# Performance work log

Measured on AMD Instinct MI355X. Metric: run time of the kernel, lower is better.

## Reference

```python
import math
import jax, jax.numpy as jnp
import numpy as np

D, NH, NL, NP = 256, 8, 3, 4
HD = D // NH
SHAPES = np.array([[92, 92], [46, 46], [23, 23]], dtype=np.int32)
LSI = np.concatenate([[0], np.cumsum(SHAPES[:, 0] * SHAPES[:, 1])[:-1]]).astype(np.int32)
LV = int((SHAPES[:, 0] * SHAPES[:, 1]).sum())  # 11109
B, LQ = 2, LV


def setup_inputs() -> dict:
    key = jax.random.key(0)
    ks = jax.random.split(key, 8)
    query = jax.random.normal(ks[0], (B, LQ, D), jnp.float32)
    reference_points = jax.random.uniform(ks[1], (B, LQ, NL, 2), dtype=jnp.float32)
    value_flat = jax.random.normal(ks[2], (B, LV, D), jnp.float32)
    # sampling_offsets: small random weight + structured directional bias (as in _reset_parameters)
    W_off = jax.random.normal(ks[3], (D, NH * NL * NP * 2), jnp.float32) * 0.01
    thetas = np.arange(NH, dtype=np.float64) * (2.0 * math.pi / NH)
    g = np.stack([np.cos(thetas), np.sin(thetas)], axis=-1)
    g = g / np.abs(g).max(axis=-1, keepdims=True)
    g = np.tile(g[:, None, None, :], (1, NL, NP, 1))
    g = g * (np.arange(NP) + 1)[None, None, :, None]
    b_off = jnp.asarray(g.reshape(-1), jnp.float32)
    W_attn = jax.random.normal(ks[4], (D, NH * NL * NP), jnp.float32) * 0.01
    b_attn = jnp.zeros((NH * NL * NP,), jnp.float32)
    W_val = jax.random.normal(ks[5], (D, D), jnp.float32) * (1.0 / math.sqrt(D))
    b_val = jnp.zeros((D,), jnp.float32)
    W_out = jax.random.normal(ks[6], (D, D), jnp.float32) * (1.0 / math.sqrt(D))
    b_out = jnp.zeros((D,), jnp.float32)
    return dict(query=query, reference_points=reference_points, value_flat=value_flat,
                W_val=W_val, b_val=b_val, W_off=W_off, b_off=b_off,
                W_attn=W_attn, b_attn=b_attn, W_out=W_out, b_out=b_out,
                spatial_shapes=jnp.asarray(SHAPES), level_start_index=jnp.asarray(LSI))


def _bilinear_sample(val_l, grid):
    """torch.F.grid_sample(mode='bilinear', padding_mode='zeros', align_corners=False).
    val_l: [B,H,W,nH,hd]; grid: [B,Q,nH,P,2] with (x,y) in [-1,1].
    Returns [B,nH,Q,P,hd]."""
    Bq, H, W, nH, hd = val_l.shape
    Q, P = grid.shape[1], grid.shape[3]
    x = ((grid[..., 0] + 1.0) * W - 1.0) * 0.5   # pixel coords, align_corners=False
    y = ((grid[..., 1] + 1.0) * H - 1.0) * 0.5
    x0f, y0f = jnp.floor(x), jnp.floor(y)
    lx, ly = x - x0f, y - y0f
    x0, y0 = x0f.astype(jnp.int32), y0f.astype(jnp.int32)
    val_bh = val_l.transpose(0, 3, 1, 2, 4).reshape(Bq * nH, H * W, hd)

    def corner(yi, xi, w):
        valid = (xi >= 0) & (xi < W) & (yi >= 0) & (yi < H)
        idx = jnp.clip(yi, 0, H - 1) * W + jnp.clip(xi, 0, W - 1)   # [B,Q,nH,P]
        idx_bh = idx.transpose(0, 2, 1, 3).reshape(Bq * nH, Q * P)
        g = jnp.take_along_axis(val_bh, idx_bh[:, :, None], axis=1)  # [B*nH, Q*P, hd]
        wm = (w * valid.astype(w.dtype)).transpose(0, 2, 1, 3).reshape(Bq * nH, Q * P, 1)
        return g * wm

    out = (corner(y0, x0, (1 - ly) * (1 - lx)) + corner(y0, x0 + 1, (1 - ly) * lx)
           + corner(y0 + 1, x0, ly * (1 - lx)) + corner(y0 + 1, x0 + 1, ly * lx))
    return out.reshape(Bq, nH, Q, P, hd)


def reference(query, reference_points, value_flat, W_val, b_val, W_off, b_off,
              W_attn, b_attn, W_out, b_out, spatial_shapes, level_start_index):
    shapes = np.asarray(spatial_shapes)          # static level geometry
    starts = np.asarray(level_start_index)
    Bq, Lq, _ = query.shape
    value = (value_flat @ W_val + b_val).reshape(Bq, -1, NH, HD)
    off = (query @ W_off + b_off).reshape(Bq, Lq, NH, NL, NP, 2)        # (dy,dx) pixels
    aw = jax.nn.softmax((query @ W_attn + b_attn).reshape(Bq, Lq, NH, NL * NP), axis=-1)
    aw = aw.reshape(Bq, Lq, NH, NL, NP)
    sh_f = jnp.asarray(shapes, jnp.float32)                              # [L,2] = (H,W)
    norm_off = off / sh_f[None, None, None, :, None, :]
    loc = reference_points[:, :, None, :, None, :] + norm_off           # [B,Lq,NH,NL,NP,2] (y,x)
    grid = 2.0 * loc[..., ::-1] - 1.0                                    # (x,y) in [-1,1]
    out = jnp.zeros((Bq, Lq, NH, HD), query.dtype)
    for l in range(NL):
        H, W = int(shapes[l, 0]), int(shapes[l, 1])
        s = int(starts[l])
        val_l = value[:, s:s + H * W].reshape(Bq, H, W, NH, HD)
        sampled = _bilinear_sample(val_l, grid[:, :, :, l])              # [B,NH,Lq,NP,HD]
        out = out + jnp.einsum('bhqpc,bqhp->bqhc', sampled, aw[:, :, :, l])
    return out.reshape(Bq, Lq, D) @ W_out + b_out
```

## Files before the change

### kernel.cpp

```cpp
#include <hip/hip_runtime.h>

#define LQn   11109
#define Bn    2
#define MTOT  (Bn * LQn)

typedef __attribute__((ext_vector_type(8))) short short8;
typedef __attribute__((ext_vector_type(4))) float f32x4;

__device__ __forceinline__ unsigned short f2bf(float f) {
  union { float f; unsigned int u; } v; v.f = f;
  unsigned int r = v.u + 0x7fffu + ((v.u >> 16) & 1u);
  return (unsigned short)(r >> 16);
}

__global__ __launch_bounds__(256) void prep_weights(
    const float* __restrict__ Wval, const float* __restrict__ Woff,
    const float* __restrict__ Wattn, const float* __restrict__ Wout,
    const float* __restrict__ boff, const float* __restrict__ battn,
    unsigned short* __restrict__ Wval_t, unsigned short* __restrict__ Wcat_t,
    unsigned short* __restrict__ Wout_t, float* __restrict__ bcat) {
  int i = blockIdx.x * 256 + threadIdx.x;
  int n = i >> 8, k = i & 255;
  if (n < 256) {
    Wval_t[i] = f2bf(Wval[k * 256 + n]);
    Wout_t[i] = f2bf(Wout[k * 256 + n]);
  }
  float src = (n < 192) ? Woff[k * 192 + n] : Wattn[k * 96 + (n - 192)];
  Wcat_t[i] = f2bf(src);
  if (i < 288) bcat[i] = (i < 192) ? boff[i] : battn[i - 192];
}

__global__ __launch_bounds__(256) void gemm_fused12(
    const float* __restrict__ Aval,
    const float* __restrict__ Aq,
    const unsigned short* __restrict__ Bval,
    const unsigned short* __restrict__ Bcat,
    const float* __restrict__ bval, const float* __restrict__ bcat,
    unsigned short* __restrict__ value16,
    float* __restrict__ logits) {
  __shared__ unsigned short As[64][40];
  __shared__ unsigned short Bs[64][40];

  const int bm = blockIdx.x;
  int bn = blockIdx.y;
  const bool is2 = bn >= 4;
  if (is2) bn -= 4;
  const float* __restrict__ A = is2 ? Aq : Aval;
  const unsigned short* __restrict__ Bt = is2 ? Bcat : Bval;
  const float* __restrict__ bias = is2 ? bcat : bval;
  const int N = is2 ? 288 : 256;

  const int t = threadIdx.x;
  const int wave = t >> 6, lane = t & 63;
  const int wm = wave >> 1, wn = wave & 1;
  const int quad = lane >> 4, l16 = lane & 15;

  const int ldr = t >> 2;
  const int ldk = (t & 3) * 8;
  const int arow = bm * 64 + ldr;
  const int brow = bn * 64 + ldr;

  f32x4 acc[2][2];
  for (int i = 0; i < 2; i++)
    for (int j = 0; j < 2; j++) acc[i][j] = (f32x4){0.f, 0.f, 0.f, 0.f};

  for (int kb = 0; kb < 8; kb++) {
    const int k0 = kb * 32;
    float4 a0 = {0.f, 0.f, 0.f, 0.f}, a1 = a0;
    uint4 bv = {0u, 0u, 0u, 0u};
    if (arow < MTOT) {
      a0 = *(const float4*)(A + (size_t)arow * 256 + k0 + ldk);
      a1 = *(const float4*)(A + (size_t)arow * 256 + k0 + ldk + 4);
    }
    if (brow < N) bv = *(const uint4*)(Bt + (size_t)brow * 256 + k0 + ldk);
    ushort4 lo, hi;
    lo.x = f2bf(a0.x); lo.y = f2bf(a0.y); lo.z = f2bf(a0.z); lo.w = f2bf(a0.w);
    hi.x = f2bf(a1.x); hi.y = f2bf(a1.y); hi.z = f2bf(a1.z); hi.w = f2bf(a1.w);
    __syncthreads();
    *(ushort4*)(&As[ldr][ldk]) = lo;
    *(ushort4*)(&As[ldr][ldk + 4]) = hi;
    *(uint4*)(&Bs[ldr][ldk]) = bv;
    __syncthreads();
    short8 af[2], bfr[2];
    for (int i = 0; i < 2; i++)
      af[i] = *(const short8*)(&As[wm * 32 + i * 16 + l16][quad * 8]);
    for (int j = 0; j < 2; j++)
      bfr[j] = *(const short8*)(&Bs[wn * 32 + j * 16 + l16][quad * 8]);
    for (int i = 0; i < 2; i++)
      for (int j = 0; j < 2; j++)
        acc[i][j] = __builtin_amdgcn_mfma_f32_16x16x32_bf16(af[i], bfr[j], acc[i][j], 0, 0, 0);
  }

  for (int i = 0; i < 2; i++)
    for (int j = 0; j < 2; j++) {
      int colg = bn * 64 + wn * 32 + j * 16 + l16;
      if (colg >= N) continue;
      float bsv = bias[colg];
      int row0 = bm * 64 + wm * 32 + i * 16 + quad * 4;
      for (int r = 0; r < 4; r++) {
        int rg = row0 + r;
        if (rg >= MTOT) continue;
        float v = acc[i][j][r] + bsv;
        if (is2) {
          logits[(size_t)rg * 288 + colg] = v;
        } else {
          int b = (rg >= LQn) ? 1 : 0;
          int p = rg - b * LQn;
          value16[((size_t)(b * 8 + (colg >> 5)) * LQn + p) * 32 + (colg & 31)] = f2bf(v);
        }
      }
    }
}

__global__ __launch_bounds__(256) void gemm_a16(
    const unsigned short* __restrict__ A,
    const unsigned short* __restrict__ Bt,
    const float* __restrict__ bias,
    float* __restrict__ C) {
  __shared__ unsigned short As[64][40];
  __shared__ unsigned short Bs[64][40];

  const int t = threadIdx.x;
  const int bm = blockIdx.x, bn = blockIdx.y;
  const int wave = t >> 6, lane = t & 63;
  const int wm = wave >> 1, wn = wave & 1;
  const int quad = lane >> 4, l16 = lane & 15;

  const int ldr = t >> 2;
  const int ldk = (t & 3) * 8;
  const int arow = bm * 64 + ldr;
  const int brow = bn * 64 + ldr;

  f32x4 acc[2][2];
  for (int i = 0; i < 2; i++)
    for (int j = 0; j < 2; j++) acc[i][j] = (f32x4){0.f, 0.f, 0.f, 0.f};

  for (int kb = 0; kb < 8; kb++) {
    const int k0 = kb * 32;
    uint4 av = {0u, 0u, 0u, 0u}, bv = {0u, 0u, 0u, 0u};
    if (arow < MTOT) av = *(const uint4*)(A + (size_t)arow * 256 + k0 + ldk);
    bv = *(const uint4*)(Bt + (size_t)brow * 256 + k0 + ldk);
    __syncthreads();
    *(uint4*)(&As[ldr][ldk]) = av;
    *(uint4*)(&Bs[ldr][ldk]) = bv;
    __syncthreads();
    short8 af[2], bfr[2];
    for (int i = 0; i < 2; i++)
      af[i] = *(const short8*)(&As[wm * 32 + i * 16 + l16][quad * 8]);
    for (int j = 0; j < 2; j++)
      bfr[j] = *(const short8*)(&Bs[wn * 32 + j * 16 + l16][quad * 8]);
    for (int i = 0; i < 2; i++)
      for (int j = 0; j < 2; j++)
        acc[i][j] = __builtin_amdgcn_mfma_f32_16x16x32_bf16(af[i], bfr[j], acc[i][j], 0, 0, 0);
  }

  for (int i = 0; i < 2; i++)
    for (int j = 0; j < 2; j++) {
      int colg = bn * 64 + wn * 32 + j * 16 + l16;
      float bsv = bias[colg];
      int row0 = bm * 64 + wm * 32 + i * 16 + quad * 4;
      for (int r = 0; r < 4; r++) {
        int rg = row0 + r;
        if (rg < MTOT) C[(size_t)rg * 256 + colg] = acc[i][j][r] + bsv;
      }
    }
}

__global__ __launch_bounds__(256) void msda_sample3(
    const unsigned short* __restrict__ value16,
    const float* __restrict__ logits,
    const float* __restrict__ refp,
    unsigned short* __restrict__ sampled) {
  __shared__ float lg[4][288];
  __shared__ float rfs[4][6];
  __shared__ float hmx[4][8], hrd[4][8];
  __shared__ float tw[4][96][4];
  __shared__ unsigned int ti[4][96][4];

  const int t = threadIdx.x;
  const int ql = t >> 6;
  const int lane = t & 63;
  const int bq = blockIdx.x * 4 + ql;
  const bool qv = bq < MTOT;

  if (qv) {
    for (int i = lane; i < 288; i += 64) lg[ql][i] = logits[(size_t)bq * 288 + i];
    if (lane < 6) rfs[ql][lane] = refp[(size_t)bq * 6 + lane];
  }
  __syncthreads();

  if (qv && lane < 8) {
    float mx = -1e30f;
#pragma unroll
    for (int i = 0; i < 12; i++) mx = fmaxf(mx, lg[ql][192 + lane * 12 + i]);
    float den = 0.f;
#pragma unroll
    for (int i = 0; i < 12; i++) den += __expf(lg[ql][192 + lane * 12 + i] - mx);
    hmx[ql][lane] = mx;
    hrd[ql][lane] = 1.0f / den;
  }
  __syncthreads();

  if (qv) {
    const int Hs[3] = {92, 46, 23};
    const int Ss[3] = {0, 8464, 10580};
#pragma unroll
    for (int rnd = 0; rnd < 2; rnd++) {
      const int s = lane + rnd * 64;
      if (s < 96) {
        const int h = s / 12;
        const int pl = s - h * 12;
        const int l = pl >> 2;
        const int H = Hs[l], W = Hs[l], S = Ss[l];
        const float aw = __expf(lg[ql][192 + s] - hmx[ql][h]) * hrd[ql][h];
        const float offy = lg[ql][2 * s], offx = lg[ql][2 * s + 1];
        const float x = rfs[ql][l * 2 + 1] * W + offx - 0.5f;
        const float y = rfs[ql][l * 2 + 0] * H + offy - 0.5f;
        const float xf = floorf(x), yf = floorf(y);
        const int x0 = (int)xf, y0 = (int)yf;
        const float lx = x - xf, ly = y - yf;
        const bool xv0 = (x0 >= 0) & (x0 < W), xv1 = (x0 + 1 >= 0) & (x0 + 1 < W);
        const bool yv0 = (y0 >= 0) & (y0 < H), yv1 = (y0 + 1 >= 0) & (y0 + 1 < H);
        const int xc0 = min(max(x0, 0), W - 1), xc1 = min(max(x0 + 1, 0), W - 1);
        const int yc0 = min(max(y0, 0), H - 1), yc1 = min(max(y0 + 1, 0), H - 1);
        ti[ql][s][0] = (unsigned)(S + yc0 * W + xc0) << 6;
        ti[ql][s][1] = (unsigned)(S + yc0 * W + xc1) << 6;
        ti[ql][s][2] = (unsigned)(S + yc1 * W + xc0) << 6;
        ti[ql][s][3] = (unsigned)(S + yc1 * W + xc1) << 6;
        tw[ql][s][0] = (yv0 & xv0) ? aw * (1.f - ly) * (1.f - lx) : 0.f;
        tw[ql][s][1] = (yv0 & xv1) ? aw * (1.f - ly) * lx : 0.f;
        tw[ql][s][2] = (yv1 & xv0) ? aw * ly * (1.f - lx) : 0.f;
        tw[ql][s][3] = (yv1 & xv1) ? aw * ly * lx : 0.f;
      }
    }
  }
  __syncthreads();

  if (qv) {
    const int h = lane >> 3, cg = lane & 7;
    const unsigned laneoff = (unsigned)h * (LQn * 64u) + (unsigned)cg * 8u;
    const char* __restrict__ vb =
        (const char*)(value16 + (size_t)(bq / LQn) * (8u * LQn * 32u));
    float a0 = 0.f, a1 = 0.f, a2 = 0.f, a3 = 0.f;
#pragma unroll
    for (int p = 0; p < 12; p++) {
      const int s = h * 12 + p;
      const f32x4 wv = *(const f32x4*)(&tw[ql][s][0]);
      const uint4 iv = *(const uint4*)(&ti[ql][s][0]);
#pragma unroll
      for (int k = 0; k < 4; k++) {
        const unsigned tib = (k == 0) ? iv.x : (k == 1) ? iv.y : (k == 2) ? iv.z : iv.w;
        const float w = wv[k];
        const uint2 u = *(const uint2*)(vb + (laneoff + tib));
        a0 += w * __uint_as_float(u.x << 16);
        a1 += w * __uint_as_float(u.x & 0xffff0000u);
        a2 += w * __uint_as_float(u.y << 16);
        a3 += w * __uint_as_float(u.y & 0xffff0000u);
      }
    }
    ushort4 o;
    o.x = f2bf(a0); o.y = f2bf(a1); o.z = f2bf(a2); o.w = f2bf(a3);
    *(ushort4*)(sampled + (size_t)bq * 256 + h * 32 + cg * 4) = o;
  }
}

extern "C" void kernel_launch(void* const* d_in, const int* in_sizes, int n_in,
                              void* d_out, int out_size, void* d_ws, size_t ws_size,
                              hipStream_t stream) {
  const float* query      = (const float*)d_in[0];
  const float* refp       = (const float*)d_in[1];
  const float* value_flat = (const float*)d_in[2];
  const float* W_val      = (const float*)d_in[3];
  const float* b_val      = (const float*)d_in[4];
  const float* W_off      = (const float*)d_in[5];
  const float* b_off      = (const float*)d_in[6];
  const float* W_attn     = (const float*)d_in[7];
  const float* b_attn     = (const float*)d_in[8];
  const float* W_out      = (const float*)d_in[9];
  const float* b_out      = (const float*)d_in[10];

  char* w = (char*)d_ws;
  size_t o = 0;
  auto carve = [&](size_t bytes) -> void* {
    void* p = (void*)(w + o);
    o += (bytes + 255) & ~(size_t)255;
    return p;
  };
  unsigned short* Wval_t  = (unsigned short*)carve(256 * 256 * 2);
  unsigned short* Wcat_t  = (unsigned short*)carve(288 * 256 * 2);
  unsigned short* Wout_t  = (unsigned short*)carve(256 * 256 * 2);
  float*          bcat    = (float*)carve(288 * 4);
  unsigned short* value16 = (unsigned short*)carve((size_t)MTOT * 256 * 2);
  float*          logits  = (float*)carve((size_t)MTOT * 288 * 4);
  unsigned short* samp_bf = (unsigned short*)carve((size_t)MTOT * 256 * 2);

  prep_weights<<<288, 256, 0, stream>>>(W_val, W_off, W_attn, W_out, b_off, b_attn,
                                        Wval_t, Wcat_t, Wout_t, bcat);

  const int mg = (MTOT + 63) / 64;
  dim3 g12(mg, 9);
  gemm_fused12<<<g12, 256, 0, stream>>>(value_flat, query, Wval_t, Wcat_t,
                                        b_val, bcat, value16, logits);

  const int sgrid = (MTOT + 3) / 4;
  msda_sample3<<<sgrid, 256, 0, stream>>>(value16, logits, refp, samp_bf);

  dim3 g3(mg, 4);
  gemm_a16<<<g3, 256, 0, stream>>>(samp_bf, Wout_t, b_out, (float*)d_out);
}
```

Baseline: 195.0 us.

## Use 128x128 GEMM tiles with direct global-to-LDS loads and a separate bf16 pre-cast

```diff
diff --git a/kernel.cpp b/kernel.cpp
--- a/kernel.cpp
+++ b/kernel.cpp
@@ -1,8 +1,7 @@
 #include <hip/hip_runtime.h>
 
 #define LQn   11109
-#define Bn    2
-#define MTOT  (Bn * LQn)
+#define MTOT  22218
 
 typedef __attribute__((ext_vector_type(8))) short short8;
 typedef __attribute__((ext_vector_type(4))) float f32x4;
@@ -11,6 +10,30 @@
   union { float f; unsigned int u; } v; v.f = f;
   unsigned int r = v.u + 0x7fffu + ((v.u >> 16) & 1u);
   return (unsigned short)(r >> 16);
+}
+
+__device__ __forceinline__ void g2l16(const void* g, void* l) {
+  __builtin_amdgcn_global_load_lds(
+      (const __attribute__((address_space(1))) unsigned int*)g,
+      (__attribute__((address_space(3))) unsigned int*)l, 16, 0, 0);
+}
+
+__global__ __launch_bounds__(256) void cast_both(
+    const float* __restrict__ q, const float* __restrict__ v,
+    unsigned short* __restrict__ qb, unsigned short* __restrict__ vb) {
+  const int n8 = MTOT * 256 / 8;
+  int i = blockIdx.x * 256 + threadIdx.x;
+  const float* src; unsigned short* dst; int j;
+  if (i < n8) { src = q; dst = qb; j = i; }
+  else        { src = v; dst = vb; j = i - n8; }
+  if (j >= n8) return;
+  float4 a = ((const float4*)src)[j * 2];
+  float4 b = ((const float4*)src)[j * 2 + 1];
+  ushort4 lo, hi;
+  lo.x = f2bf(a.x); lo.y = f2bf(a.y); lo.z = f2bf(a.z); lo.w = f2bf(a.w);
+  hi.x = f2bf(b.x); hi.y = f2bf(b.y); hi.z = f2bf(b.z); hi.w = f2bf(b.w);
+  ((ushort4*)dst)[j * 2] = lo;
+  ((ushort4*)dst)[j * 2 + 1] = hi;
 }
 
 __global__ __launch_bounds__(256) void prep_weights(
@@ -25,145 +48,140 @@
     Wval_t[i] = f2bf(Wval[k * 256 + n]);
     Wout_t[i] = f2bf(Wout[k * 256 + n]);
   }
-  float src = (n < 192) ? Woff[k * 192 + n] : Wattn[k * 96 + (n - 192)];
+  float src = (n < 192) ? Woff[k * 192 + n] : (n < 288 ? Wattn[k * 96 + (n - 192)] : 0.f);
   Wcat_t[i] = f2bf(src);
-  if (i < 288) bcat[i] = (i < 192) ? boff[i] : battn[i - 192];
-}
-
-__global__ __launch_bounds__(256) void gemm_fused12(
-    const float* __restrict__ Aval,
-    const float* __restrict__ Aq,
-    const unsigned short* __restrict__ Bval,
-    const unsigned short* __restrict__ Bcat,
+  if (i < 384) bcat[i] = (i < 192) ? boff[i] : (i < 288 ? battn[i - 192] : 0.f);
+}
+
+__device__ __forceinline__ void gemm128_loop(
+    const unsigned short* __restrict__ A, int Arow0,
+    const unsigned short* __restrict__ Bt, int Brow0,
+    unsigned short* As, unsigned short* Bs, f32x4 (&acc)[4][4]) {
+  const int t = threadIdx.x;
+  const int w = t >> 6, lane = t & 63;
+  const int rowl = lane >> 2;
+  const int kby = (lane & 3) * 16;
+  const int quad = lane >> 4, l16 = lane & 15;
+  const int wm = w >> 1, wn = w & 1;
+
+#pragma unroll 1
+  for (int kb = 0; kb < 8; kb++) {
+    if (kb) __syncthreads();
+#pragma unroll
+    for (int i16 = 0; i16 < 2; i16++) {
+      int r = w * 32 + i16 * 16 + rowl;
+      int ga = Arow0 + r; ga = (ga < MTOT) ? ga : (MTOT - 1);
+      g2l16((const char*)A + (size_t)ga * 512 + kb * 64 + kby,
+            (char*)As + w * 2048 + i16 * 1024);
+      g2l16((const char*)Bt + (size_t)(Brow0 + r) * 512 + kb * 64 + kby,
+            (char*)Bs + w * 2048 + i16 * 1024);
+    }
+    __syncthreads();
+    short8 af[4], bfr[4];
+#pragma unroll
+    for (int i = 0; i < 4; i++)
+      af[i] = *(const short8*)((const char*)As + (wm * 64 + i * 16 + l16) * 64 + quad * 16);
+#pragma unroll
+    for (int j = 0; j < 4; j++)
+      bfr[j] = *(const short8*)((const char*)Bs + (wn * 64 + j * 16 + l16) * 64 + quad * 16);
+#pragma unroll
+    for (int i = 0; i < 4; i++)
+#pragma unroll
+      for (int j = 0; j < 4; j++)
+        acc[i][j] = __builtin_amdgcn_mfma_f32_16x16x32_bf16(af[i], bfr[j], acc[i][j], 0, 0, 0);
+  }
+}
+
+__global__ __launch_bounds__(256) void gemm128_12(
+    const unsigned short* __restrict__ Av, const unsigned short* __restrict__ Aq,
+    const unsigned short* __restrict__ Bv, const unsigned short* __restrict__ Bc,
     const float* __restrict__ bval, const float* __restrict__ bcat,
-    unsigned short* __restrict__ value16,
-    float* __restrict__ logits) {
-  __shared__ unsigned short As[64][40];
-  __shared__ unsigned short Bs[64][40];
-
+    unsigned short* __restrict__ value16, float* __restrict__ logits) {
+  __shared__ unsigned short As[128 * 32];
+  __shared__ unsigned short Bs[128 * 32];
   const int bm = blockIdx.x;
-  int bn = blockIdx.y;
-  const bool is2 = bn >= 4;
-  if (is2) bn -= 4;
-  const float* __restrict__ A = is2 ? Aq : Aval;
-  const unsigned short* __restrict__ Bt = is2 ? Bcat : Bval;
-  const float* __restrict__ bias = is2 ? bcat : bval;
-  const int N = is2 ? 288 : 256;
-
-  const int t = threadIdx.x;
-  const int wave = t >> 6, lane = t & 63;
-  const int wm = wave >> 1, wn = wave & 1;
+  const int bn = blockIdx.y;
+  const bool is2 = bn >= 2;
+  const int bnl = is2 ? bn - 2 : bn;
+
+  f32x4 acc[4][4];
+  for (int i = 0; i < 4; i++)
+    for (int j = 0; j < 4; j++) acc[i][j] = (f32x4){0.f, 0.f, 0.f, 0.f};
+
+  gemm128_loop(is2 ? Aq : Av, bm * 128, is2 ? Bc : Bv, bnl * 128, As, Bs, acc);
+
+  const int t = threadIdx.x, lane = t & 63;
   const int quad = lane >> 4, l16 = lane & 15;
-
-  const int ldr = t >> 2;
-  const int ldk = (t & 3) * 8;
-  const int arow = bm * 64 + ldr;
-  const int brow = bn * 64 + ldr;
-
-  f32x4 acc[2][2];
-  for (int i = 0; i < 2; i++)
-    for (int j = 0; j < 2; j++) acc[i][j] = (f32x4){0.f, 0.f, 0.f, 0.f};
-
-  for (int kb = 0; kb < 8; kb++) {
-    const int k0 = kb * 32;
-    float4 a0 = {0.f, 0.f, 0.f, 0.f}, a1 = a0;
-    uint4 bv = {0u, 0u, 0u, 0u};
-    if (arow < MTOT) {
-      a0 = *(const float4*)(A + (size_t)arow * 256 + k0 + ldk);
-      a1 = *(const float4*)(A + (size_t)arow * 256 + k0 + ldk + 4);
-    }
-    if (brow < N) bv = *(const uint4*)(Bt + (size_t)brow * 256 + k0 + ldk);
-    ushort4 lo, hi;
-    lo.x = f2bf(a0.x); lo.y = f2bf(a0.y); lo.z = f2bf(a0.z); lo.w = f2bf(a0.w);
-    hi.x = f2bf(a1.x); hi.y = f2bf(a1.y); hi.z = f2bf(a1.z); hi.w = f2bf(a1.w);
-    __syncthreads();
-    *(ushort4*)(&As[ldr][ldk]) = lo;
-    *(ushort4*)(&As[ldr][ldk + 4]) = hi;
-    *(uint4*)(&Bs[ldr][ldk]) = bv;
-    __syncthreads();
-    short8 af[2], bfr[2];
-    for (int i = 0; i < 2; i++)
-      af[i] = *(const short8*)(&As[wm * 32 + i * 16 + l16][quad * 8]);
-    for (int j = 0; j < 2; j++)
-      bfr[j] = *(const short8*)(&Bs[wn * 32 + j * 16 + l16][quad * 8]);
-    for (int i = 0; i < 2; i++)
-      for (int j = 0; j < 2; j++)
-        acc[i][j] = __builtin_amdgcn_mfma_f32_16x16x32_bf16(af[i], bfr[j], acc[i][j], 0, 0, 0);
-  }
-
-  for (int i = 0; i < 2; i++)
-    for (int j = 0; j < 2; j++) {
-      int colg = bn * 64 + wn * 32 + j * 16 + l16;
-      if (colg >= N) continue;
-      float bsv = bias[colg];
-      int row0 = bm * 64 + wm * 32 + i * 16 + quad * 4;
+  const int wm = t >> 7, wn = (t >> 6) & 1;
+
+  if (!is2) {
+#pragma unroll
+    for (int j = 0; j < 4; j++) {
+      const int col = bnl * 128 + wn * 64 + j * 16 + l16;
+      const float bs = bval[col];
+      const int hbase = col >> 5, cch = col & 31;
+#pragma unroll
+      for (int i = 0; i < 4; i++) {
+        const int row0 = bm * 128 + wm * 64 + i * 16 + quad * 4;
+#pragma unroll
+        for (int r = 0; r < 4; r++) {
+          const int rg = row0 + r;
+          if (rg >= MTOT) continue;
+          const int b = rg >= LQn ? 1 : 0;
+          const int p = rg - b * LQn;
+          value16[((size_t)(b * 8 + hbase) * LQn + p) * 32 + cch] = f2bf(acc[i][j][r] + bs);
+        }
+      }
+    }
+  } else {
+#pragma unroll
+    for (int j = 0; j < 4; j++) {
+      const int col = bnl * 128 + wn * 64 + j * 16 + l16;
+      if (col >= 288) continue;
+      const float bs = bcat[col];
+#pragma unroll
+      for (int i = 0; i < 4; i++) {
+        const int row0 = bm * 128 + wm * 64 + i * 16 + quad * 4;
+#pragma unroll
+        for (int r = 0; r < 4; r++) {
+          const int rg = row0 + r;
+          if (rg < MTOT) logits[(size_t)rg * 288 + col] = acc[i][j][r] + bs;
+        }
+      }
+    }
+  }
+}
+
+__global__ __launch_bounds__(256) void gemm128_out(
+    const unsigned short* __restrict__ A, const unsigned short* __restrict__ Bt,
+    const float* __restrict__ bias, float* __restrict__ C) {
+  __shared__ unsigned short As[128 * 32];
+  __shared__ unsigned short Bs[128 * 32];
+  const int bm = blockIdx.x, bn = blockIdx.y;
+
+  f32x4 acc[4][4];
+  for (int i = 0; i < 4; i++)
+    for (int j = 0; j < 4; j++) acc[i][j] = (f32x4){0.f, 0.f, 0.f, 0.f};
+
+  gemm128_loop(A, bm * 128, Bt, bn * 128, As, Bs, acc);
+
+  const int t = threadIdx.x, lane = t & 63;
+  const int quad = lane >> 4, l16 = lane & 15;
+  const int wm = t >> 7, wn = (t >> 6) & 1;
+#pragma unroll
+  for (int j = 0; j < 4; j++) {
+    const int col = bn * 128 + wn * 64 + j * 16 + l16;
+    const float bs = bias[col];
+#pragma unroll
+    for (int i = 0; i < 4; i++) {
+      const int row0 = bm * 128 + wm * 64 + i * 16 + quad * 4;
+#pragma unroll
       for (int r = 0; r < 4; r++) {
-        int rg = row0 + r;
-        if (rg >= MTOT) continue;
-        float v = acc[i][j][r] + bsv;
-        if (is2) {
-          logits[(size_t)rg * 288 + colg] = v;
-        } else {
-          int b = (rg >= LQn) ? 1 : 0;
-          int p = rg - b * LQn;
-          value16[((size_t)(b * 8 + (colg >> 5)) * LQn + p) * 32 + (colg & 31)] = f2bf(v);
-        }
-      }
-    }
-}
-
-__global__ __launch_bounds__(256) void gemm_a16(
-    const unsigned short* __restrict__ A,
-    const unsigned short* __restrict__ Bt,
-    const float* __restrict__ bias,
-    float* __restrict__ C) {
-  __shared__ unsigned short As[64][40];
-  __shared__ unsigned short Bs[64][40];
-
-  const int t = threadIdx.x;
-  const int bm = blockIdx.x, bn = blockIdx.y;
-  const int wave = t >> 6, lane = t & 63;
-  const int wm = wave >> 1, wn = wave & 1;
-  const int quad = lane >> 4, l16 = lane & 15;
-
-  const int ldr = t >> 2;
-  const int ldk = (t & 3) * 8;
-  const int arow = bm * 64 + ldr;
-  const int brow = bn * 64 + ldr;
-
-  f32x4 acc[2][2];
-  for (int i = 0; i < 2; i++)
-    for (int j = 0; j < 2; j++) acc[i][j] = (f32x4){0.f, 0.f, 0.f, 0.f};
-
-  for (int kb = 0; kb < 8; kb++) {
-    const int k0 = kb * 32;
-    uint4 av = {0u, 0u, 0u, 0u}, bv = {0u, 0u, 0u, 0u};
-    if (arow < MTOT) av = *(const uint4*)(A + (size_t)arow * 256 + k0 + ldk);
-    bv = *(const uint4*)(Bt + (size_t)brow * 256 + k0 + ldk);
-    __syncthreads();
-    *(uint4*)(&As[ldr][ldk]) = av;
-    *(uint4*)(&Bs[ldr][ldk]) = bv;
-    __syncthreads();
-    short8 af[2], bfr[2];
-    for (int i = 0; i < 2; i++)
-      af[i] = *(const short8*)(&As[wm * 32 + i * 16 + l16][quad * 8]);
-    for (int j = 0; j < 2; j++)
-      bfr[j] = *(const short8*)(&Bs[wn * 32 + j * 16 + l16][quad * 8]);
-    for (int i = 0; i < 2; i++)
-      for (int j = 0; j < 2; j++)
-        acc[i][j] = __builtin_amdgcn_mfma_f32_16x16x32_bf16(af[i], bfr[j], acc[i][j], 0, 0, 0);
-  }
-
-  for (int i = 0; i < 2; i++)
-    for (int j = 0; j < 2; j++) {
-      int colg = bn * 64 + wn * 32 + j * 16 + l16;
-      float bsv = bias[colg];
-      int row0 = bm * 64 + wm * 32 + i * 16 + quad * 4;
-      for (int r = 0; r < 4; r++) {
-        int rg = row0 + r;
-        if (rg < MTOT) C[(size_t)rg * 256 + colg] = acc[i][j][r] + bsv;
-      }
-    }
+        const int rg = row0 + r;
+        if (rg < MTOT) C[(size_t)rg * 256 + col] = acc[i][j][r] + bs;
+      }
+    }
+  }
 }
 
 __global__ __launch_bounds__(256) void msda_sample3(
@@ -286,25 +304,29 @@
     o += (bytes + 255) & ~(size_t)255;
     return p;
   };
+  unsigned short* q_bf    = (unsigned short*)carve((size_t)MTOT * 256 * 2);
+  unsigned short* v_bf    = (unsigned short*)carve((size_t)MTOT * 256 * 2);
   unsigned short* Wval_t  = (unsigned short*)carve(256 * 256 * 2);
-  unsigned short* Wcat_t  = (unsigned short*)carve(288 * 256 * 2);
+  unsigned short* Wcat_t  = (unsigned short*)carve(384 * 256 * 2);
   unsigned short* Wout_t  = (unsigned short*)carve(256 * 256 * 2);
-  float*          bcat    = (float*)carve(288 * 4);
+  float*          bcat    = (float*)carve(384 * 4);
   unsigned short* value16 = (unsigned short*)carve((size_t)MTOT * 256 * 2);
   float*          logits  = (float*)carve((size_t)MTOT * 288 * 4);
   unsigned short* samp_bf = (unsigned short*)carve((size_t)MTOT * 256 * 2);
 
-  prep_weights<<<288, 256, 0, stream>>>(W_val, W_off, W_attn, W_out, b_off, b_attn,
+  const int n8x2 = 2 * (MTOT * 256 / 8);
+  cast_both<<<(n8x2 + 255) / 256, 256, 0, stream>>>(query, value_flat, q_bf, v_bf);
+  prep_weights<<<384, 256, 0, stream>>>(W_val, W_off, W_attn, W_out, b_off, b_attn,
                                         Wval_t, Wcat_t, Wout_t, bcat);
 
-  const int mg = (MTOT + 63) / 64;
-  dim3 g12(mg, 9);
-  gemm_fused12<<<g12, 256, 0, stream>>>(value_flat, query, Wval_t, Wcat_t,
-                                        b_val, bcat, value16, logits);
+  const int mg = (MTOT + 127) / 128;
+  dim3 g12(mg, 5);
+  gemm128_12<<<g12, 256, 0, stream>>>(v_bf, q_bf, Wval_t, Wcat_t,
+                                      b_val, bcat, value16, logits);
 
   const int sgrid = (MTOT + 3) / 4;
   msda_sample3<<<sgrid, 256, 0, stream>>>(value16, logits, refp, samp_bf);
 
-  dim3 g3(mg, 4);
-  gemm_a16<<<g3, 256, 0, stream>>>(samp_bf, Wout_t, b_out, (float*)d_out);
-}
+  dim3 g3(mg, 2);
+  gemm128_out<<<g3, 256, 0, stream>>>(samp_bf, Wout_t, b_out, (float*)d_out);
+}
```

Measured after the change: 204.8 us. 5.1% more time.

## Process eight queries per block with 16-byte gathers and spread sampling setup

Applied to the files above, without the earlier changes.

```diff
diff --git a/kernel.cpp b/kernel.cpp
--- a/kernel.cpp
+++ b/kernel.cpp
@@ -1,8 +1,7 @@
 #include <hip/hip_runtime.h>
 
 #define LQn   11109
-#define Bn    2
-#define MTOT  (Bn * LQn)
+#define MTOT  22218
 
 typedef __attribute__((ext_vector_type(8))) short short8;
 typedef __attribute__((ext_vector_type(4))) float f32x4;
@@ -166,56 +165,58 @@
     }
 }
 
-__global__ __launch_bounds__(256) void msda_sample3(
+__global__ __launch_bounds__(256) void msda_sample4(
     const unsigned short* __restrict__ value16,
     const float* __restrict__ logits,
     const float* __restrict__ refp,
     unsigned short* __restrict__ sampled) {
-  __shared__ float lg[4][288];
-  __shared__ float rfs[4][6];
-  __shared__ float hmx[4][8], hrd[4][8];
-  __shared__ float tw[4][96][4];
-  __shared__ unsigned int ti[4][96][4];
+  __shared__ float          tw[8][96][4];
+  __shared__ unsigned short ti[8][96][4];
+  __shared__ float hmx[8][8], hrd[8][8];
+  __shared__ float rfs[8][6];
 
   const int t = threadIdx.x;
-  const int ql = t >> 6;
-  const int lane = t & 63;
-  const int bq = blockIdx.x * 4 + ql;
-  const bool qv = bq < MTOT;
-
-  if (qv) {
-    for (int i = lane; i < 288; i += 64) lg[ql][i] = logits[(size_t)bq * 288 + i];
-    if (lane < 6) rfs[ql][lane] = refp[(size_t)bq * 6 + lane];
+  const int qbase = blockIdx.x * 8;
+
+  if (t < 48) {
+    int q = t / 6;
+    if (qbase + q < MTOT) rfs[q][t - q * 6] = refp[(size_t)qbase * 6 + t];
+  }
+  if (t >= 64 && t < 128) {
+    int tt = t - 64;
+    int q = tt >> 3, h = tt & 7;
+    int bq = qbase + q;
+    if (bq < MTOT) {
+      const float* lrow = logits + (size_t)bq * 288 + 192 + h * 12;
+      float mx = -1e30f;
+#pragma unroll
+      for (int i = 0; i < 12; i++) mx = fmaxf(mx, lrow[i]);
+      float den = 0.f;
+#pragma unroll
+      for (int i = 0; i < 12; i++) den += __expf(lrow[i] - mx);
+      hmx[q][h] = mx;
+      hrd[q][h] = 1.0f / den;
+    }
   }
   __syncthreads();
 
-  if (qv && lane < 8) {
-    float mx = -1e30f;
-#pragma unroll
-    for (int i = 0; i < 12; i++) mx = fmaxf(mx, lg[ql][192 + lane * 12 + i]);
-    float den = 0.f;
-#pragma unroll
-    for (int i = 0; i < 12; i++) den += __expf(lg[ql][192 + lane * 12 + i] - mx);
-    hmx[ql][lane] = mx;
-    hrd[ql][lane] = 1.0f / den;
-  }
-  __syncthreads();
-
-  if (qv) {
+  {
     const int Hs[3] = {92, 46, 23};
     const int Ss[3] = {0, 8464, 10580};
 #pragma unroll
-    for (int rnd = 0; rnd < 2; rnd++) {
-      const int s = lane + rnd * 64;
-      if (s < 96) {
-        const int h = s / 12;
-        const int pl = s - h * 12;
+    for (int r = 0; r < 3; r++) {
+      const int task = t + r * 256;
+      const int q = task / 96, s = task - q * 96;
+      const int bq = qbase + q;
+      if (bq < MTOT) {
+        const int h = s / 12, pl = s - h * 12;
         const int l = pl >> 2;
         const int H = Hs[l], W = Hs[l], S = Ss[l];
-        const float aw = __expf(lg[ql][192 + s] - hmx[ql][h]) * hrd[ql][h];
-        const float offy = lg[ql][2 * s], offx = lg[ql][2 * s + 1];
-        const float x = rfs[ql][l * 2 + 1] * W + offx - 0.5f;
-        const float y = rfs[ql][l * 2 + 0] * H + offy - 0.5f;
+        const float* lrow = logits + (size_t)bq * 288;
+        const float aw = __expf(lrow[192 + s] - hmx[q][h]) * hrd[q][h];
+        const float offy = lrow[2 * s], offx = lrow[2 * s + 1];
+        const float x = rfs[q][l * 2 + 1] * W + offx - 0.5f;
+        const float y = rfs[q][l * 2 + 0] * H + offy - 0.5f;
         const float xf = floorf(x), yf = floorf(y);
         const int x0 = (int)xf, y0 = (int)yf;
         const float lx = x - xf, ly = y - yf;
@@ -223,44 +224,62 @@
         const bool yv0 = (y0 >= 0) & (y0 < H), yv1 = (y0 + 1 >= 0) & (y0 + 1 < H);
         const int xc0 = min(max(x0, 0), W - 1), xc1 = min(max(x0 + 1, 0), W - 1);
         const int yc0 = min(max(y0, 0), H - 1), yc1 = min(max(y0 + 1, 0), H - 1);
-        ti[ql][s][0] = (unsigned)(S + yc0 * W + xc0) << 6;
-        ti[ql][s][1] = (unsigned)(S + yc0 * W + xc1) << 6;
-        ti[ql][s][2] = (unsigned)(S + yc1 * W + xc0) << 6;
-        ti[ql][s][3] = (unsigned)(S + yc1 * W + xc1) << 6;
-        tw[ql][s][0] = (yv0 & xv0) ? aw * (1.f - ly) * (1.f - lx) : 0.f;
-        tw[ql][s][1] = (yv0 & xv1) ? aw * (1.f - ly) * lx : 0.f;
-        tw[ql][s][2] = (yv1 & xv0) ? aw * ly * (1.f - lx) : 0.f;
-        tw[ql][s][3] = (yv1 & xv1) ? aw * ly * lx : 0.f;
+        const int slot = pl * 8 + h;
+        ti[q][slot][0] = (unsigned short)(S + yc0 * W + xc0);
+        ti[q][slot][1] = (unsigned short)(S + yc0 * W + xc1);
+        ti[q][slot][2] = (unsigned short)(S + yc1 * W + xc0);
+        ti[q][slot][3] = (unsigned short)(S + yc1 * W + xc1);
+        tw[q][slot][0] = (yv0 & xv0) ? aw * (1.f - ly) * (1.f - lx) : 0.f;
+        tw[q][slot][1] = (yv0 & xv1) ? aw * (1.f - ly) * lx : 0.f;
+        tw[q][slot][2] = (yv1 & xv0) ? aw * ly * (1.f - lx) : 0.f;
+        tw[q][slot][3] = (yv1 & xv1) ? aw * ly * lx : 0.f;
       }
     }
   }
   __syncthreads();
 
-  if (qv) {
-    const int h = lane >> 3, cg = lane & 7;
-    const unsigned laneoff = (unsigned)h * (LQn * 64u) + (unsigned)cg * 8u;
+  {
+    const int w = t >> 6, lane = t & 63;
+    const int q = w * 2 + (lane >> 5);
+    const int h = (lane >> 2) & 7, cg = lane & 3;
+    const int bq = qbase + q;
+    const bool qv = bq < MTOT;
+    const int bqc = qv ? bq : 0;
     const char* __restrict__ vb =
-        (const char*)(value16 + (size_t)(bq / LQn) * (8u * LQn * 32u));
+        (const char*)value16 + (size_t)(bqc / LQn) * ((size_t)LQn * 512);
+    const unsigned laneoff = (unsigned)h * (LQn * 64u) + (unsigned)cg * 16u;
+
     float a0 = 0.f, a1 = 0.f, a2 = 0.f, a3 = 0.f;
+    float a4 = 0.f, a5 = 0.f, a6 = 0.f, a7 = 0.f;
 #pragma unroll
     for (int p = 0; p < 12; p++) {
-      const int s = h * 12 + p;
-      const f32x4 wv = *(const f32x4*)(&tw[ql][s][0]);
-      const uint4 iv = *(const uint4*)(&ti[ql][s][0]);
+      const int slot = p * 8 + h;
+      const ushort4 tiv = *(const ushort4*)(&ti[q][slot][0]);
+      const f32x4 wv = *(const f32x4*)(&tw[q][slot][0]);
 #pragma unroll
       for (int k = 0; k < 4; k++) {
-        const unsigned tib = (k == 0) ? iv.x : (k == 1) ? iv.y : (k == 2) ? iv.z : iv.w;
-        const float w = wv[k];
-        const uint2 u = *(const uint2*)(vb + (laneoff + tib));
-        a0 += w * __uint_as_float(u.x << 16);
-        a1 += w * __uint_as_float(u.x & 0xffff0000u);
-        a2 += w * __uint_as_float(u.y << 16);
-        a3 += w * __uint_as_float(u.y & 0xffff0000u);
+        const unsigned pix =
+            (k == 0) ? tiv.x : (k == 1) ? tiv.y : (k == 2) ? tiv.z : tiv.w;
+        const float wgt = wv[k];
+        const uint4 u = *(const uint4*)(vb + ((pix << 6) + laneoff));
+        a0 += wgt * __uint_as_float(u.x << 16);
+        a1 += wgt * __uint_as_float(u.x & 0xffff0000u);
+        a2 += wgt * __uint_as_float(u.y << 16);
+        a3 += wgt * __uint_as_float(u.y & 0xffff0000u);
+        a4 += wgt * __uint_as_float(u.z << 16);
+        a5 += wgt * __uint_as_float(u.z & 0xffff0000u);
+        a6 += wgt * __uint_as_float(u.w << 16);
+        a7 += wgt * __uint_as_float(u.w & 0xffff0000u);
       }
     }
-    ushort4 o;
-    o.x = f2bf(a0); o.y = f2bf(a1); o.z = f2bf(a2); o.w = f2bf(a3);
-    *(ushort4*)(sampled + (size_t)bq * 256 + h * 32 + cg * 4) = o;
+    if (qv) {
+      uint4 o;
+      o.x = (unsigned)f2bf(a0) | ((unsigned)f2bf(a1) << 16);
+      o.y = (unsigned)f2bf(a2) | ((unsigned)f2bf(a3) << 16);
+      o.z = (unsigned)f2bf(a4) | ((unsigned)f2bf(a5) << 16);
+      o.w = (unsigned)f2bf(a6) | ((unsigned)f2bf(a7) << 16);
+      *(uint4*)(sampled + (size_t)bq * 256 + h * 32 + cg * 8) = o;
+    }
   }
 }
 
@@ -302,8 +321,8 @@
   gemm_fused12<<<g12, 256, 0, stream>>>(value_flat, query, Wval_t, Wcat_t,
                                         b_val, bcat, value16, logits);
 
-  const int sgrid = (MTOT + 3) / 4;
-  msda_sample3<<<sgrid, 256, 0, stream>>>(value16, logits, refp, samp_bf);
+  const int sgrid = (MTOT + 7) / 8;
+  msda_sample4<<<sgrid, 256, 0, stream>>>(value16, logits, refp, samp_bf);
 
   dim3 g3(mg, 4);
   gemm_a16<<<g3, 256, 0, stream>>>(samp_bf, Wout_t, b_out, (float*)d_out);
```

Result: faster. 190.7 us (-2.2%).
